# Kernel tuning notes

Hardware: AMD Instinct MI355X
Metric: run time of the kernel (lower is better)

## Reference

```python
import jax, jax.numpy as jnp
import numpy as np

KERNEL_SIZE = 10
CHANNELS = 3
MEAN = (KERNEL_SIZE - 1) // 2  # 4


def setup_inputs() -> dict:
    key = jax.random.key(0)
    x = jax.random.uniform(key, (32, CHANNELS, 512, 512), dtype=jnp.float32)
    return {"x": x}


def reference(x) -> jnp.ndarray:
    # (1 - x) * 0.5, then replicate pad by MEAN on H and W
    y = (1.0 - x) * 0.5
    y = jnp.pad(y, ((0, 0), (0, 0), (MEAN, MEAN), (MEAN, MEAN)), mode="edge")
    # depthwise (groups=channels) conv with all-ones 10x10 kernel, VALID padding
    # weight layout OIHW with O=CHANNELS, I=1 (feature_group_count=CHANNELS)
    w = jnp.ones((CHANNELS, 1, KERNEL_SIZE, KERNEL_SIZE), dtype=x.dtype)
    out = jax.lax.conv_general_dilated(
        y, w,
        window_strides=(1, 1),
        padding="VALID",
        dimension_numbers=("NCHW", "OIHW", "NCHW"),
        feature_group_count=CHANNELS,
    )
    return out  # [B, C, H-1, W-1]
```

## Files before the change

kernel.cpp:

```cpp
#include <hip/hip_runtime.h>


#define IMG 512
#define OUTW 511
#define KS 10
#define MEAN 4
#define SUBB 16
#define TS (SUBB + KS - 1)
#define ROWF4 (IMG / 4)
#define NF4 (TS * ROWF4)
#define NTHREADS 512
#define NBANDS (IMG / SUBB)
#define NIMG 96
#define NWG (NBANDS * NIMG)
#define CPX (NWG / 8)

__global__ __launch_bounds__(NTHREADS) void onedilate_kernel(
    const float* __restrict__ x, float* __restrict__ out)
{
    __shared__ float smemf[TS * IMG];

    const int lin = blockIdx.y * NBANDS + blockIdx.x;
    const int swz = (lin & 7) * CPX + (lin >> 3);
    const int bx  = swz & (NBANDS - 1);
    const int bc  = swz >> 5;

    const int tid = threadIdx.x;
    const int rb  = bx * SUBB;

    const float* __restrict__ xim = x + (size_t)bc * (IMG * IMG);
    float* __restrict__ oim = out + (size_t)bc * (OUTW * OUTW);

#define STAGE(idx_)                                                        \
    {                                                                      \
        const int r_  = (idx_) >> 7;                                       \
        const int c4_ = (idx_) & (ROWF4 - 1);                              \
        const int ri_ = min(max(rb - MEAN + r_, 0), IMG - 1);              \
        __builtin_amdgcn_global_load_lds(                                  \
            (const __attribute__((address_space(1))) void*)                \
                (xim + (size_t)ri_ * IMG + c4_ * 4),                       \
            (__attribute__((address_space(3))) void*)(smemf + (idx_) * 4), \
            16, 0, 0);                                                     \
    }
#pragma unroll
    for (int k = 0; k < 6; ++k) STAGE(k * NTHREADS + tid)
    if (tid < (NF4 - 6 * NTHREADS)) STAGE(6 * NTHREADS + tid)
#undef STAGE
    __syncthreads();

    const int j  = tid & 127;
    const int rg = tid >> 7;
    const int cbase = 4 * j;
    const int bl0 = max(cbase - 4, 0);
    const int bl2 = min(cbase + 4, IMG - 4);
    const int bl3 = min(cbase + 8, IMG - 4);
    const bool lo0 = (cbase - 4 < 0);
    const bool hi2 = (cbase + 4 > IMG - 4);
    const bool hi3 = (cbase + 8 > IMG - 4);

    const float* sf = smemf;
    float4 a0 = make_float4(0.f, 0.f, 0.f, 0.f);
    float4 a1 = a0, a2 = a0, a3 = a0;

#define ACC4(A) { A.x += H.x; A.y += H.y; A.z += H.z; A.w += H.w; }

#pragma unroll
    for (int sl = 0; sl < 13; ++sl) {
        const int s = rg * 4 + sl;
        const float* rp = sf + s * IMG;
        float4 v0 = *(const float4*)(rp + bl0);
        float4 v1 = *(const float4*)(rp + cbase);
        float4 v2 = *(const float4*)(rp + bl2);
        float4 v3 = *(const float4*)(rp + bl3);
        if (lo0) v0 = make_float4(v0.x, v0.x, v0.x, v0.x);
        if (hi2) v2 = make_float4(v2.w, v2.w, v2.w, v2.w);
        const float w12 = hi3 ? v3.w : v3.x;

        const float S = ((v0.x + v0.y) + (v0.z + v0.w))
                      + ((v1.x + v1.y) + (v1.z + v1.w))
                      + (v2.x + v2.y);
        const float d1  = v2.z - v0.x;
        const float d2  = v2.w - v0.y;
        const float d3  = w12  - v0.z;
        const float d12 = d1 + d2;
        float4 H;
        H.x = S;
        H.y = S + d1;
        H.z = S + d12;
        H.w = S + (d12 + d3);

        if (sl <= 9)             ACC4(a0)
        if (sl >= 1 && sl <= 10) ACC4(a1)
        if (sl >= 2 && sl <= 11) ACC4(a2)
        if (sl >= 3)             ACC4(a3)
    }
#undef ACC4

    const int i0 = rb + rg * 4;
#define STORE(ro, A)                                                       \
    { const int i = i0 + (ro);                                             \
      if (i < OUTW) {                                                      \
          float* op = oim + (size_t)i * OUTW + cbase;                      \
          op[0] = fmaf(A.x, -0.5f, 50.0f);                                 \
          op[1] = fmaf(A.y, -0.5f, 50.0f);                                 \
          op[2] = fmaf(A.z, -0.5f, 50.0f);                                 \
          if (cbase + 3 < OUTW) op[3] = fmaf(A.w, -0.5f, 50.0f);           \
      } }
    STORE(0, a0)
    STORE(1, a1)
    STORE(2, a2)
    STORE(3, a3)
#undef STORE
}

extern "C" void kernel_launch(void* const* d_in, const int* in_sizes, int n_in,
                              void* d_out, int out_size, void* d_ws, size_t ws_size,
                              hipStream_t stream) {
    const float* x = (const float*)d_in[0];
    float* out = (float*)d_out;

    dim3 block(NTHREADS, 1, 1);
    dim3 grid(NBANDS, NIMG, 1);
    onedilate_kernel<<<grid, block, 0, stream>>>(x, out);
}
```

Measured before the change: 175.9 us.

## Make kernel persistent over images with double-buffered LDS prefetch

Shrinks the grid from 96 images × 32 bands to 8 image groups × 32 bands. Each block now loops over 12 images and prefetches the next image's band tile into a second LDS buffer while it computes the current one. The goal is to overlap global loads with compute and stores, and to amortize block launch cost. In exchange it doubles LDS use per block, which may reduce occupancy. It also leaves only 256 blocks, which lowers parallelism and latency hiding on a large GPU.

```diff
diff --git a/kernel.cpp b/kernel.cpp
--- a/kernel.cpp
+++ b/kernel.cpp
@@ -9,44 +9,24 @@
 #define TS (SUBB + KS - 1)
 #define ROWF4 (IMG / 4)
 #define NF4 (TS * ROWF4)
+#define TILEF (TS * IMG)
 #define NTHREADS 512
 #define NBANDS (IMG / SUBB)
-#define NIMG 96
-#define NWG (NBANDS * NIMG)
-#define CPX (NWG / 8)
+#define NIG 8
+#define TPB 12
 
 __global__ __launch_bounds__(NTHREADS) void onedilate_kernel(
     const float* __restrict__ x, float* __restrict__ out)
 {
-    __shared__ float smemf[TS * IMG];
+    __shared__ float smemf[2 * TILEF];
 
     const int lin = blockIdx.y * NBANDS + blockIdx.x;
-    const int swz = (lin & 7) * CPX + (lin >> 3);
+    const int swz = (lin & 7) * 32 + (lin >> 3);
     const int bx  = swz & (NBANDS - 1);
-    const int bc  = swz >> 5;
+    const int ig  = swz >> 5;
 
     const int tid = threadIdx.x;
     const int rb  = bx * SUBB;
-
-    const float* __restrict__ xim = x + (size_t)bc * (IMG * IMG);
-    float* __restrict__ oim = out + (size_t)bc * (OUTW * OUTW);
-
-#define STAGE(idx_)                                                        \
-    {                                                                      \
-        const int r_  = (idx_) >> 7;                                       \
-        const int c4_ = (idx_) & (ROWF4 - 1);                              \
-        const int ri_ = min(max(rb - MEAN + r_, 0), IMG - 1);              \
-        __builtin_amdgcn_global_load_lds(                                  \
-            (const __attribute__((address_space(1))) void*)                \
-                (xim + (size_t)ri_ * IMG + c4_ * 4),                       \
-            (__attribute__((address_space(3))) void*)(smemf + (idx_) * 4), \
-            16, 0, 0);                                                     \
-    }
-#pragma unroll
-    for (int k = 0; k < 6; ++k) STAGE(k * NTHREADS + tid)
-    if (tid < (NF4 - 6 * NTHREADS)) STAGE(6 * NTHREADS + tid)
-#undef STAGE
-    __syncthreads();
 
     const int j  = tid & 127;
     const int rg = tid >> 7;
@@ -58,59 +38,105 @@
     const bool hi2 = (cbase + 4 > IMG - 4);
     const bool hi3 = (cbase + 8 > IMG - 4);
 
-    const float* sf = smemf;
-    float4 a0 = make_float4(0.f, 0.f, 0.f, 0.f);
-    float4 a1 = a0, a2 = a0, a3 = a0;
+#define STAGE1(buf_, xim_, idx_)                                           \
+    {                                                                      \
+        const int r_  = (idx_) >> 7;                                       \
+        const int c4_ = (idx_) & (ROWF4 - 1);                              \
+        const int ri_ = min(max(rb - MEAN + r_, 0), IMG - 1);              \
+        __builtin_amdgcn_global_load_lds(                                  \
+            (const __attribute__((address_space(1))) void*)                \
+                ((xim_) + (size_t)ri_ * IMG + c4_ * 4),                    \
+            (__attribute__((address_space(3))) void*)                      \
+                (smemf + (buf_) * TILEF + (idx_) * 4),                     \
+            16, 0, 0);                                                     \
+    }
+#define STAGE(buf_, xim_)                                                  \
+    {                                                                      \
+        _Pragma("unroll")                                                  \
+        for (int k = 0; k < 6; ++k) STAGE1(buf_, xim_, k * NTHREADS + tid) \
+        if (tid < (NF4 - 6 * NTHREADS)) STAGE1(buf_, xim_, 6 * NTHREADS + tid) \
+    }
+#define DRAIN_BARRIER()                                                    \
+    {                                                                      \
+        asm volatile("s_waitcnt vmcnt(0)" ::: "memory");                   \
+        __builtin_amdgcn_sched_barrier(0);                                 \
+        __builtin_amdgcn_s_barrier();                                      \
+    }
+
+    {
+        const float* xim0 = x + (size_t)(ig * TPB) * (IMG * IMG);
+        STAGE(0, xim0)
+    }
+    DRAIN_BARRIER()
+
+    int cur = 0;
+#pragma unroll 1
+    for (int t = 0; t < TPB; ++t) {
+        if (t + 1 < TPB) {
+            const float* xnext = x + (size_t)(ig * TPB + t + 1) * (IMG * IMG);
+            STAGE(cur ^ 1, xnext)
+        }
+
+        const float* sf = smemf + cur * TILEF;
+        float4 a0 = make_float4(0.f, 0.f, 0.f, 0.f);
+        float4 a1 = a0, a2 = a0, a3 = a0;
 
 #define ACC4(A) { A.x += H.x; A.y += H.y; A.z += H.z; A.w += H.w; }
+#pragma unroll
+        for (int sl = 0; sl < 13; ++sl) {
+            const int s = rg * 4 + sl;
+            const float* rp = sf + s * IMG;
+            float4 v0 = *(const float4*)(rp + bl0);
+            float4 v1 = *(const float4*)(rp + cbase);
+            float4 v2 = *(const float4*)(rp + bl2);
+            float4 v3 = *(const float4*)(rp + bl3);
+            if (lo0) v0 = make_float4(v0.x, v0.x, v0.x, v0.x);
+            if (hi2) v2 = make_float4(v2.w, v2.w, v2.w, v2.w);
+            const float w12 = hi3 ? v3.w : v3.x;
 
-#pragma unroll
-    for (int sl = 0; sl < 13; ++sl) {
-        const int s = rg * 4 + sl;
-        const float* rp = sf + s * IMG;
-        float4 v0 = *(const float4*)(rp + bl0);
-        float4 v1 = *(const float4*)(rp + cbase);
-        float4 v2 = *(const float4*)(rp + bl2);
-        float4 v3 = *(const float4*)(rp + bl3);
-        if (lo0) v0 = make_float4(v0.x, v0.x, v0.x, v0.x);
-        if (hi2) v2 = make_float4(v2.w, v2.w, v2.w, v2.w);
-        const float w12 = hi3 ? v3.w : v3.x;
+            const float S = ((v0.x + v0.y) + (v0.z + v0.w))
+                          + ((v1.x + v1.y) + (v1.z + v1.w))
+                          + (v2.x + v2.y);
+            const float d1  = v2.z - v0.x;
+            const float d2  = v2.w - v0.y;
+            const float d3  = w12  - v0.z;
+            const float d12 = d1 + d2;
+            float4 H;
+            H.x = S;
+            H.y = S + d1;
+            H.z = S + d12;
+            H.w = S + (d12 + d3);
 
-        const float S = ((v0.x + v0.y) + (v0.z + v0.w))
-                      + ((v1.x + v1.y) + (v1.z + v1.w))
-                      + (v2.x + v2.y);
-        const float d1  = v2.z - v0.x;
-        const float d2  = v2.w - v0.y;
-        const float d3  = w12  - v0.z;
-        const float d12 = d1 + d2;
-        float4 H;
-        H.x = S;
-        H.y = S + d1;
-        H.z = S + d12;
-        H.w = S + (d12 + d3);
-
-        if (sl <= 9)             ACC4(a0)
-        if (sl >= 1 && sl <= 10) ACC4(a1)
-        if (sl >= 2 && sl <= 11) ACC4(a2)
-        if (sl >= 3)             ACC4(a3)
-    }
+            if (sl <= 9)             ACC4(a0)
+            if (sl >= 1 && sl <= 10) ACC4(a1)
+            if (sl >= 2 && sl <= 11) ACC4(a2)
+            if (sl >= 3)             ACC4(a3)
+        }
 #undef ACC4
 
-    const int i0 = rb + rg * 4;
+        float* oim = out + (size_t)(ig * TPB + t) * (OUTW * OUTW);
+        const int i0 = rb + rg * 4;
 #define STORE(ro, A)                                                       \
-    { const int i = i0 + (ro);                                             \
-      if (i < OUTW) {                                                      \
-          float* op = oim + (size_t)i * OUTW + cbase;                      \
-          op[0] = fmaf(A.x, -0.5f, 50.0f);                                 \
-          op[1] = fmaf(A.y, -0.5f, 50.0f);                                 \
-          op[2] = fmaf(A.z, -0.5f, 50.0f);                                 \
-          if (cbase + 3 < OUTW) op[3] = fmaf(A.w, -0.5f, 50.0f);           \
-      } }
-    STORE(0, a0)
-    STORE(1, a1)
-    STORE(2, a2)
-    STORE(3, a3)
+        { const int i = i0 + (ro);                                         \
+          if (i < OUTW) {                                                  \
+              float* op = oim + (size_t)i * OUTW + cbase;                  \
+              op[0] = fmaf(A.x, -0.5f, 50.0f);                             \
+              op[1] = fmaf(A.y, -0.5f, 50.0f);                             \
+              op[2] = fmaf(A.z, -0.5f, 50.0f);                             \
+              if (cbase + 3 < OUTW) op[3] = fmaf(A.w, -0.5f, 50.0f);       \
+          } }
+        STORE(0, a0)
+        STORE(1, a1)
+        STORE(2, a2)
+        STORE(3, a3)
 #undef STORE
+
+        DRAIN_BARRIER()
+        cur ^= 1;
+    }
+#undef STAGE
+#undef STAGE1
+#undef DRAIN_BARRIER
 }
 
 extern "C" void kernel_launch(void* const* d_in, const int* in_sizes, int n_in,
@@ -120,6 +146,6 @@
     float* out = (float*)d_out;
 
     dim3 block(NTHREADS, 1, 1);
-    dim3 grid(NBANDS, NIMG, 1);
+    dim3 grid(NBANDS, NIG, 1);
     onedilate_kernel<<<grid, block, 0, stream>>>(x, out);
 }
```

Measured after the change: 181.8 us. +3.4%, slower.

## Make blocks persistent over six images with separable vertical-then-horizontal box sum

Applied to the files above, without the earlier changes.

Each of 256 workgroups of 1024 threads now handles a 32-row band across six consecutive images. For each image it computes vertical 10-row sums into a second shared buffer with a sliding window, then does the horizontal sum from that buffer. While the horizontal pass and stores run, it starts the async global-to-LDS load of the next image's tile. This is meant to cut the redundant 13-row horizontal work and the halo overhead, and to overlap loads with compute. The cost is roughly 120KB of dynamic LDS (so one block per CU), fewer total blocks, and extra barriers.

```diff
diff --git a/kernel.cpp b/kernel.cpp
--- a/kernel.cpp
+++ b/kernel.cpp
@@ -5,52 +5,46 @@
 #define OUTW 511
 #define KS 10
 #define MEAN 4
-#define SUBB 16
+#define SUBB 32
 #define TS (SUBB + KS - 1)
 #define ROWF4 (IMG / 4)
-#define NF4 (TS * ROWF4)
-#define NTHREADS 512
+#define TF4 (TS * ROWF4)
+#define TILEF (TS * IMG)
+#define VF (SUBB * IMG)
+#define SMEM_BYTES ((TILEF + VF) * 4)
+#define NTHREADS 1024
 #define NBANDS (IMG / SUBB)
-#define NIMG 96
-#define NWG (NBANDS * NIMG)
-#define CPX (NWG / 8)
+#define TPB 6
+
+__device__ __forceinline__ float4 f4add(float4 a, float4 b) {
+    return make_float4(a.x + b.x, a.y + b.y, a.z + b.z, a.w + b.w);
+}
+__device__ __forceinline__ float4 f4slide(float4 v, float4 add, float4 sub) {
+    return make_float4(v.x + add.x - sub.x, v.y + add.y - sub.y,
+                       v.z + add.z - sub.z, v.w + add.w - sub.w);
+}
 
 __global__ __launch_bounds__(NTHREADS) void onedilate_kernel(
     const float* __restrict__ x, float* __restrict__ out)
 {
-    __shared__ float smemf[TS * IMG];
+    extern __shared__ float smem[];
+    float* Tb = smem;
+    float* Vb = smem + TILEF;
 
-    const int lin = blockIdx.y * NBANDS + blockIdx.x;
-    const int swz = (lin & 7) * CPX + (lin >> 3);
-    const int bx  = swz & (NBANDS - 1);
-    const int bc  = swz >> 5;
+    const int lin   = blockIdx.x;
+    const int xcd   = lin & 7;
+    const int slot  = lin >> 3;
+    const int band  = slot & (NBANDS - 1);
+    const int ihalf = slot >> 4;
+    const int img0  = xcd * 12 + ihalf * TPB;
+    const int rb    = band * SUBB;
 
     const int tid = threadIdx.x;
-    const int rb  = bx * SUBB;
+    const int jc  = tid & (ROWF4 - 1);
+    const int rg  = tid >> 7;
+    const int vr0 = rg * 4;
 
-    const float* __restrict__ xim = x + (size_t)bc * (IMG * IMG);
-    float* __restrict__ oim = out + (size_t)bc * (OUTW * OUTW);
-
-#define STAGE(idx_)                                                        \
-    {                                                                      \
-        const int r_  = (idx_) >> 7;                                       \
-        const int c4_ = (idx_) & (ROWF4 - 1);                              \
-        const int ri_ = min(max(rb - MEAN + r_, 0), IMG - 1);              \
-        __builtin_amdgcn_global_load_lds(                                  \
-            (const __attribute__((address_space(1))) void*)                \
-                (xim + (size_t)ri_ * IMG + c4_ * 4),                       \
-            (__attribute__((address_space(3))) void*)(smemf + (idx_) * 4), \
-            16, 0, 0);                                                     \
-    }
-#pragma unroll
-    for (int k = 0; k < 6; ++k) STAGE(k * NTHREADS + tid)
-    if (tid < (NF4 - 6 * NTHREADS)) STAGE(6 * NTHREADS + tid)
-#undef STAGE
-    __syncthreads();
-
-    const int j  = tid & 127;
-    const int rg = tid >> 7;
-    const int cbase = 4 * j;
+    const int cbase = 4 * jc;
     const int bl0 = max(cbase - 4, 0);
     const int bl2 = min(cbase + 4, IMG - 4);
     const int bl3 = min(cbase + 8, IMG - 4);
@@ -58,59 +52,97 @@
     const bool hi2 = (cbase + 4 > IMG - 4);
     const bool hi3 = (cbase + 8 > IMG - 4);
 
-    const float* sf = smemf;
-    float4 a0 = make_float4(0.f, 0.f, 0.f, 0.f);
-    float4 a1 = a0, a2 = a0, a3 = a0;
+#define STAGE1(xim_, idx_)                                                 \
+    {                                                                      \
+        const int r_  = (idx_) >> 7;                                       \
+        const int c4_ = (idx_) & (ROWF4 - 1);                              \
+        const int ri_ = min(max(rb - MEAN + r_, 0), IMG - 1);              \
+        __builtin_amdgcn_global_load_lds(                                  \
+            (const __attribute__((address_space(1))) void*)                \
+                ((xim_) + (size_t)ri_ * IMG + c4_ * 4),                    \
+            (__attribute__((address_space(3))) void*)(Tb + (idx_) * 4),    \
+            16, 0, 0);                                                     \
+    }
+#define STAGE(xim_)                                                        \
+    {                                                                      \
+        _Pragma("unroll")                                                  \
+        for (int k = 0; k < 5; ++k) STAGE1(xim_, k * NTHREADS + tid)       \
+        if (tid < (TF4 - 5 * NTHREADS)) STAGE1(xim_, 5 * NTHREADS + tid)   \
+    }
 
-#define ACC4(A) { A.x += H.x; A.y += H.y; A.z += H.z; A.w += H.w; }
+    STAGE(x + (size_t)img0 * (IMG * IMG))
+    __syncthreads();
 
+#pragma unroll 1
+    for (int t = 0; t < TPB; ++t) {
+        {
+            const float4* Tv = (const float4*)Tb;
+            float4* Vv = (float4*)Vb;
+            const float4 t0  = Tv[(vr0 + 0) * ROWF4 + jc];
+            const float4 t1  = Tv[(vr0 + 1) * ROWF4 + jc];
+            const float4 t2  = Tv[(vr0 + 2) * ROWF4 + jc];
+            const float4 t3  = Tv[(vr0 + 3) * ROWF4 + jc];
+            const float4 t4  = Tv[(vr0 + 4) * ROWF4 + jc];
+            const float4 t5  = Tv[(vr0 + 5) * ROWF4 + jc];
+            const float4 t6  = Tv[(vr0 + 6) * ROWF4 + jc];
+            const float4 t7  = Tv[(vr0 + 7) * ROWF4 + jc];
+            const float4 t8  = Tv[(vr0 + 8) * ROWF4 + jc];
+            const float4 t9  = Tv[(vr0 + 9) * ROWF4 + jc];
+            const float4 t10 = Tv[(vr0 + 10) * ROWF4 + jc];
+            const float4 t11 = Tv[(vr0 + 11) * ROWF4 + jc];
+            const float4 t12 = Tv[(vr0 + 12) * ROWF4 + jc];
+            float4 v = f4add(f4add(f4add(f4add(t0, t1), f4add(t2, t3)),
+                                   f4add(f4add(t4, t5), f4add(t6, t7))),
+                             f4add(t8, t9));
+            Vv[(vr0 + 0) * ROWF4 + jc] = v;
+            v = f4slide(v, t10, t0);
+            Vv[(vr0 + 1) * ROWF4 + jc] = v;
+            v = f4slide(v, t11, t1);
+            Vv[(vr0 + 2) * ROWF4 + jc] = v;
+            v = f4slide(v, t12, t2);
+            Vv[(vr0 + 3) * ROWF4 + jc] = v;
+        }
+        __syncthreads();
+
+        if (t + 1 < TPB) STAGE(x + (size_t)(img0 + t + 1) * (IMG * IMG))
+
+        {
+            float* oim = out + (size_t)(img0 + t) * (OUTW * OUTW);
 #pragma unroll
-    for (int sl = 0; sl < 13; ++sl) {
-        const int s = rg * 4 + sl;
-        const float* rp = sf + s * IMG;
-        float4 v0 = *(const float4*)(rp + bl0);
-        float4 v1 = *(const float4*)(rp + cbase);
-        float4 v2 = *(const float4*)(rp + bl2);
-        float4 v3 = *(const float4*)(rp + bl3);
-        if (lo0) v0 = make_float4(v0.x, v0.x, v0.x, v0.x);
-        if (hi2) v2 = make_float4(v2.w, v2.w, v2.w, v2.w);
-        const float w12 = hi3 ? v3.w : v3.x;
+            for (int k = 0; k < 4; ++k) {
+                const int r = vr0 + k;
+                const float* rp = Vb + r * IMG;
+                float4 v0 = *(const float4*)(rp + bl0);
+                float4 v1 = *(const float4*)(rp + cbase);
+                float4 v2 = *(const float4*)(rp + bl2);
+                float4 v3 = *(const float4*)(rp + bl3);
+                if (lo0) v0 = make_float4(v0.x, v0.x, v0.x, v0.x);
+                if (hi2) v2 = make_float4(v2.w, v2.w, v2.w, v2.w);
+                const float w12 = hi3 ? v3.w : v3.x;
 
-        const float S = ((v0.x + v0.y) + (v0.z + v0.w))
-                      + ((v1.x + v1.y) + (v1.z + v1.w))
-                      + (v2.x + v2.y);
-        const float d1  = v2.z - v0.x;
-        const float d2  = v2.w - v0.y;
-        const float d3  = w12  - v0.z;
-        const float d12 = d1 + d2;
-        float4 H;
-        H.x = S;
-        H.y = S + d1;
-        H.z = S + d12;
-        H.w = S + (d12 + d3);
+                const float S = ((v0.x + v0.y) + (v0.z + v0.w))
+                              + ((v1.x + v1.y) + (v1.z + v1.w))
+                              + (v2.x + v2.y);
+                const float d1  = v2.z - v0.x;
+                const float d2  = v2.w - v0.y;
+                const float d3  = w12  - v0.z;
+                const float d12 = d1 + d2;
 
-        if (sl <= 9)             ACC4(a0)
-        if (sl >= 1 && sl <= 10) ACC4(a1)
-        if (sl >= 2 && sl <= 11) ACC4(a2)
-        if (sl >= 3)             ACC4(a3)
+                const int i = rb + r;
+                if (i < OUTW) {
+                    float* op = oim + (size_t)i * OUTW + cbase;
+                    op[0] = fmaf(S, -0.5f, 50.0f);
+                    op[1] = fmaf(S + d1, -0.5f, 50.0f);
+                    op[2] = fmaf(S + d12, -0.5f, 50.0f);
+                    if (cbase + 3 < OUTW)
+                        op[3] = fmaf(S + (d12 + d3), -0.5f, 50.0f);
+                }
+            }
+        }
+        __syncthreads();
     }
-#undef ACC4
-
-    const int i0 = rb + rg * 4;
-#define STORE(ro, A)                                                       \
-    { const int i = i0 + (ro);                                             \
-      if (i < OUTW) {                                                      \
-          float* op = oim + (size_t)i * OUTW + cbase;                      \
-          op[0] = fmaf(A.x, -0.5f, 50.0f);                                 \
-          op[1] = fmaf(A.y, -0.5f, 50.0f);                                 \
-          op[2] = fmaf(A.z, -0.5f, 50.0f);                                 \
-          if (cbase + 3 < OUTW) op[3] = fmaf(A.w, -0.5f, 50.0f);           \
-      } }
-    STORE(0, a0)
-    STORE(1, a1)
-    STORE(2, a2)
-    STORE(3, a3)
-#undef STORE
+#undef STAGE
+#undef STAGE1
 }
 
 extern "C" void kernel_launch(void* const* d_in, const int* in_sizes, int n_in,
@@ -119,7 +151,15 @@
     const float* x = (const float*)d_in[0];
     float* out = (float*)d_out;
 
+    static bool attr_set = false;
+    if (!attr_set) {
+        hipFuncSetAttribute((const void*)onedilate_kernel,
+                            hipFuncAttributeMaxDynamicSharedMemorySize,
+                            SMEM_BYTES);
+        attr_set = true;
+    }
+
     dim3 block(NTHREADS, 1, 1);
-    dim3 grid(NBANDS, NIMG, 1);
-    onedilate_kernel<<<grid, block, 0, stream>>>(x, out);
+    dim3 grid(256, 1, 1);
+    onedilate_kernel<<<grid, block, SMEM_BYTES, stream>>>(x, out);
 }
```

Measured after the change: 180.1 us. 1.02x slower.

## Halve row band per workgroup and use vectorized float4 output stores

Applied to the files above, without the earlier changes.

Shrinks each workgroup's row band from 16 to 8 output rows. Each thread now accumulates 2 output rows from 11 staged LDS rows instead of 4 rows from 13, and the image-index swizzle shift is adjusted to match. The smaller LDS tile allows more resident workgroups per CU and gives a larger grid. The cost is more halo re-reading, both from global memory and from LDS, per output row. Output stores become single float4 writes where possible, even though rows of width 511 leave those addresses unaligned to 16 bytes.

```diff
diff --git a/kernel.cpp b/kernel.cpp
--- a/kernel.cpp
+++ b/kernel.cpp
@@ -5,7 +5,7 @@
 #define OUTW 511
 #define KS 10
 #define MEAN 4
-#define SUBB 16
+#define SUBB 8
 #define TS (SUBB + KS - 1)
 #define ROWF4 (IMG / 4)
 #define NF4 (TS * ROWF4)
@@ -23,7 +23,7 @@
     const int lin = blockIdx.y * NBANDS + blockIdx.x;
     const int swz = (lin & 7) * CPX + (lin >> 3);
     const int bx  = swz & (NBANDS - 1);
-    const int bc  = swz >> 5;
+    const int bc  = swz >> 6;
 
     const int tid = threadIdx.x;
     const int rb  = bx * SUBB;
@@ -31,7 +31,7 @@
     const float* __restrict__ xim = x + (size_t)bc * (IMG * IMG);
     float* __restrict__ oim = out + (size_t)bc * (OUTW * OUTW);
 
-#define STAGE(idx_)                                                        \
+#define STAGE1(idx_)                                                       \
     {                                                                      \
         const int r_  = (idx_) >> 7;                                       \
         const int c4_ = (idx_) & (ROWF4 - 1);                              \
@@ -43,9 +43,9 @@
             16, 0, 0);                                                     \
     }
 #pragma unroll
-    for (int k = 0; k < 6; ++k) STAGE(k * NTHREADS + tid)
-    if (tid < (NF4 - 6 * NTHREADS)) STAGE(6 * NTHREADS + tid)
-#undef STAGE
+    for (int k = 0; k < 4; ++k) STAGE1(k * NTHREADS + tid)
+    if (tid < (NF4 - 4 * NTHREADS)) STAGE1(4 * NTHREADS + tid)
+#undef STAGE1
     __syncthreads();
 
     const int j  = tid & 127;
@@ -58,16 +58,13 @@
     const bool hi2 = (cbase + 4 > IMG - 4);
     const bool hi3 = (cbase + 8 > IMG - 4);
 
-    const float* sf = smemf;
-    float4 a0 = make_float4(0.f, 0.f, 0.f, 0.f);
-    float4 a1 = a0, a2 = a0, a3 = a0;
-
-#define ACC4(A) { A.x += H.x; A.y += H.y; A.z += H.z; A.w += H.w; }
+    const int base = 2 * rg;
+    float4 A0 = make_float4(0.f, 0.f, 0.f, 0.f);
+    float4 A1 = A0;
 
 #pragma unroll
-    for (int sl = 0; sl < 13; ++sl) {
-        const int s = rg * 4 + sl;
-        const float* rp = sf + s * IMG;
+    for (int k = 0; k < 11; ++k) {
+        const float* rp = smemf + (base + k) * IMG;
         float4 v0 = *(const float4*)(rp + bl0);
         float4 v1 = *(const float4*)(rp + cbase);
         float4 v2 = *(const float4*)(rp + bl2);
@@ -89,27 +86,27 @@
         H.z = S + d12;
         H.w = S + (d12 + d3);
 
-        if (sl <= 9)             ACC4(a0)
-        if (sl >= 1 && sl <= 10) ACC4(a1)
-        if (sl >= 2 && sl <= 11) ACC4(a2)
-        if (sl >= 3)             ACC4(a3)
+        if (k <= 9) { A0.x += H.x; A0.y += H.y; A0.z += H.z; A0.w += H.w; }
+        if (k >= 1) { A1.x += H.x; A1.y += H.y; A1.z += H.z; A1.w += H.w; }
     }
-#undef ACC4
 
-    const int i0 = rb + rg * 4;
-#define STORE(ro, A)                                                       \
-    { const int i = i0 + (ro);                                             \
-      if (i < OUTW) {                                                      \
+    const int i0 = rb + 2 * rg;
+#define STORE(ro_, A_)                                                     \
+    { const int i = i0 + (ro_);                                            \
+      if (i < OUTW) {                      \
           float* op = oim + (size_t)i * OUTW + cbase;                      \
-          op[0] = fmaf(A.x, -0.5f, 50.0f);                                 \
-          op[1] = fmaf(A.y, -0.5f, 50.0f);                                 \
-          op[2] = fmaf(A.z, -0.5f, 50.0f);                                 \
-          if (cbase + 3 < OUTW) op[3] = fmaf(A.w, -0.5f, 50.0f);           \
+          const float4 o = make_float4(fmaf(A_.x, -0.5f, 50.0f),           \
+                                       fmaf(A_.y, -0.5f, 50.0f),           \
+                                       fmaf(A_.z, -0.5f, 50.0f),           \
+                                       fmaf(A_.w, -0.5f, 50.0f));          \
+          if (cbase + 3 < OUTW) {                                          \
+              *(float4*)op = o;                   \
+          } else {                               \
+              op[0] = o.x; op[1] = o.y; op[2] = o.z;                       \
+          }                                                                \
       } }
-    STORE(0, a0)
-    STORE(1, a1)
-    STORE(2, a2)
-    STORE(3, a3)
+    STORE(0, A0)
+    STORE(1, A1)
 #undef STORE
 }
 
```

After: 177.5 us. Within noise of the previous version (+0.9%).
